# Optimization experiments

Hardware: AMD Instinct MI355X
Metric: run time of the kernel (lower is better)

Reference implementation:

```python
import jax, jax.numpy as jnp
import numpy as np

EMBED_DIM = 768
NUM_HEADS = 12
D_K = EMBED_DIM // NUM_HEADS
FFN_DIM = 3072
N_QUBITS = 8
LN_EPS = 1e-5


def layer_norm(x, g, b):
    mu = jnp.mean(x, axis=-1, keepdims=True)
    var = jnp.mean(jnp.square(x - mu), axis=-1, keepdims=True)
    return (x - mu) * jax.lax.rsqrt(var + LN_EPS) * g + b


def setup_inputs() -> dict:
    key = jax.random.key(0)
    ks = jax.random.split(key, 8)
    B, S = 4, 2048
    s_comb = 1.0 / np.sqrt(EMBED_DIM)
    s_w1 = 1.0 / np.sqrt(N_QUBITS)
    s_w2 = 1.0 / np.sqrt(FFN_DIM)
    return {
        "x": jax.random.normal(ks[0], (B, S, EMBED_DIM), jnp.float32),
        "combine_w": jax.random.uniform(ks[1], (EMBED_DIM, EMBED_DIM), jnp.float32, -s_comb, s_comb),
        "theta": jax.random.normal(ks[2], (N_QUBITS,), jnp.float32),
        "w1": jax.random.uniform(ks[3], (FFN_DIM, N_QUBITS), jnp.float32, -s_w1, s_w1),
        "w2": jax.random.uniform(ks[4], (EMBED_DIM, FFN_DIM), jnp.float32, -s_w2, s_w2),
        "ln1_g": jnp.ones((EMBED_DIM,), jnp.float32),
        "ln1_b": jnp.zeros((EMBED_DIM,), jnp.float32),
        "ln2_g": jnp.ones((EMBED_DIM,), jnp.float32),
        "ln2_b": jnp.zeros((EMBED_DIM,), jnp.float32),
    }


def reference(x, combine_w, theta, w1, w2, ln1_g, ln1_b, ln2_g, ln2_b):
    B, S, D = x.shape
    # --- attention (q = k = v = x split into heads; QLayer is never used in forward) ---
    xh = x.reshape(B, S, NUM_HEADS, D_K).transpose(0, 2, 1, 3)  # [B,H,S,dk]
    scores = jnp.einsum("bhqd,bhkd->bhqk", xh, xh) / jnp.sqrt(jnp.asarray(D_K, x.dtype))
    probs = jax.nn.softmax(scores, axis=-1)
    attn = jnp.einsum("bhqk,bhkd->bhqd", probs, xh)
    attn = attn.transpose(0, 2, 1, 3).reshape(B, S, D)
    attn_out = attn @ combine_w.T
    # --- residual + norm1 ---
    h = layer_norm(x + attn_out, ln1_g, ln1_b)
    # --- quantum FFN: RX(x_i) then RY(theta_i) per wire, <Z_i> = cos(x_i)*cos(theta_i) ---
    meas = jnp.cos(h[..., :N_QUBITS]) * jnp.cos(theta)  # [B,S,nq]
    ffn = jax.nn.relu(meas @ w1.T) @ w2.T               # [B,S,D]
    # --- residual + norm2 ---
    return layer_norm(h + ffn, ln2_g, ln2_b)
```

## Files before the change

kernel.cpp:

```cpp
#include <hip/hip_runtime.h>
#include <math.h>


#define B_    4
#define S_    2048
#define D_    768
#define H_    12
#define DK_   64
#define FFN_  3072
#define NQ_   8
#define M_    (B_ * S_)

typedef __attribute__((ext_vector_type(8))) short bf16x8;
typedef __attribute__((ext_vector_type(4))) float f32x4;

static __device__ __forceinline__ unsigned short f2bf(float f) {
    unsigned u = __float_as_uint(f);
    unsigned r = (u + 0x7FFFu + ((u >> 16) & 1u)) >> 16;
    return (unsigned short)r;
}
static __device__ __forceinline__ unsigned pk2(float a, float b) {
    return (unsigned)f2bf(a) | ((unsigned)f2bf(b) << 16);
}
static __device__ __forceinline__ bf16x8 pack8(float4 a, float4 b) {
    bf16x8 r;
    r[0] = (short)f2bf(a.x); r[1] = (short)f2bf(a.y);
    r[2] = (short)f2bf(a.z); r[3] = (short)f2bf(a.w);
    r[4] = (short)f2bf(b.x); r[5] = (short)f2bf(b.y);
    r[6] = (short)f2bf(b.z); r[7] = (short)f2bf(b.w);
    return r;
}

__global__ __launch_bounds__(256, 2)
void attn_mfma(const float* __restrict__ x, unsigned short* __restrict__ attnb)
{
    __shared__ __align__(16) short Ks[64 * 64];
    __shared__ __align__(16) short Vt[64 * 64];
    __shared__ __align__(16) short Ps[4 * 32 * 64];

    const int tid = threadIdx.x;
    const int w   = tid >> 6;
    const int l   = tid & 63;
    const int g   = l >> 4;
    const int l15 = l & 15;

    const int q0 = blockIdx.x * 128;
    const int hh = blockIdx.y;
    const int bb = blockIdx.z;

    const float* xh = x + ((size_t)bb * S_) * D_ + hh * DK_;

    bf16x8 qf[2][2];
    {
        const float* xq = xh + (size_t)(q0 + w * 32) * D_;
        #pragma unroll
        for (int qt = 0; qt < 2; ++qt)
            #pragma unroll
            for (int ks = 0; ks < 2; ++ks) {
                const float* p = xq + (size_t)(qt * 16 + l15) * D_ + ks * 32 + g * 8;
                float4 f0 = *reinterpret_cast<const float4*>(p);
                float4 f1 = *reinterpret_cast<const float4*>(p + 4);
                qf[qt][ks] = pack8(f0, f1);
            }
    }

    f32x4 oacc[2][4];
    float mrun[2][4], lrun[2][4];
    #pragma unroll
    for (int qt = 0; qt < 2; ++qt)
        #pragma unroll
        for (int i = 0; i < 4; ++i) {
            oacc[qt][i] = (f32x4){0.f, 0.f, 0.f, 0.f};
            mrun[qt][i] = -3.0e38f; lrun[qt][i] = 0.f;
        }

    short* Pw = Ps + w * 32 * 64;

    for (int kt = 0; kt < S_ / 64; ++kt) {
        __syncthreads();
        const float* xk = xh + (size_t)(kt * 64) * D_;

        #pragma unroll
        for (int it = 0; it < 2; ++it) {
            int c = tid + it * 256;
            int r = c >> 3, b = c & 7;
            const float* p = xk + (size_t)r * D_ + b * 8;
            float4 f0 = *reinterpret_cast<const float4*>(p);
            float4 f1 = *reinterpret_cast<const float4*>(p + 4);
            *reinterpret_cast<bf16x8*>(&Ks[r * 64 + ((b ^ (r & 7)) << 3)]) = pack8(f0, f1);
        }
        {
            int kv0 = (tid & 31) * 2;
            int dch = tid >> 5;
            unsigned* Vt32 = reinterpret_cast<unsigned*>(Vt);
            #pragma unroll
            for (int dp = 0; dp < 2; ++dp) {
                int d0 = dp * 32 + dch * 4;
                float4 fa = *reinterpret_cast<const float4*>(xk + (size_t)kv0 * D_ + d0);
                float4 fb = *reinterpret_cast<const float4*>(xk + (size_t)(kv0 + 1) * D_ + d0);
                const float* pa = reinterpret_cast<const float*>(&fa);
                const float* pb = reinterpret_cast<const float*>(&fb);
                #pragma unroll
                for (int j = 0; j < 4; ++j) {
                    int d = d0 + j;
                    Vt32[d * 32 + ((kv0 >> 1) ^ ((d & 7) << 2))] = pk2(pa[j], pb[j]);
                }
            }
        }
        __syncthreads();

        f32x4 sacc[2][4];
        #pragma unroll
        for (int qt = 0; qt < 2; ++qt)
            #pragma unroll
            for (int kj = 0; kj < 4; ++kj) sacc[qt][kj] = (f32x4){0.f, 0.f, 0.f, 0.f};

        #pragma unroll
        for (int ks = 0; ks < 2; ++ks) {
            bf16x8 kf[4];
            #pragma unroll
            for (int kj = 0; kj < 4; ++kj) {
                int r = kj * 16 + l15;
                kf[kj] = *reinterpret_cast<const bf16x8*>(
                    &Ks[r * 64 + (((ks * 4 + g) ^ (r & 7)) << 3)]);
            }
            #pragma unroll
            for (int qt = 0; qt < 2; ++qt)
                #pragma unroll
                for (int kj = 0; kj < 4; ++kj)
                    sacc[qt][kj] = __builtin_amdgcn_mfma_f32_16x16x32_bf16(
                        qf[qt][ks], kf[kj], sacc[qt][kj], 0, 0, 0);
        }

        #pragma unroll
        for (int qt = 0; qt < 2; ++qt) {
            #pragma unroll
            for (int reg = 0; reg < 4; ++reg) {
                float s0 = sacc[qt][0][reg] * 0.125f;
                float s1 = sacc[qt][1][reg] * 0.125f;
                float s2 = sacc[qt][2][reg] * 0.125f;
                float s3 = sacc[qt][3][reg] * 0.125f;
                float mx = fmaxf(fmaxf(s0, s1), fmaxf(s2, s3));
                #pragma unroll
                for (int msk = 1; msk < 16; msk <<= 1) mx = fmaxf(mx, __shfl_xor(mx, msk));
                float mnew = fmaxf(mrun[qt][reg], mx);
                float corr = __expf(mrun[qt][reg] - mnew);
                mrun[qt][reg] = mnew;
                float p0 = __expf(s0 - mnew), p1 = __expf(s1 - mnew);
                float p2 = __expf(s2 - mnew), p3 = __expf(s3 - mnew);
                float ps = (p0 + p1) + (p2 + p3);
                #pragma unroll
                for (int msk = 1; msk < 16; msk <<= 1) ps += __shfl_xor(ps, msk);
                lrun[qt][reg] = lrun[qt][reg] * corr + ps;
                #pragma unroll
                for (int dt = 0; dt < 4; ++dt) oacc[qt][dt][reg] *= corr;
                int q = qt * 16 + g * 4 + reg;
                short* pr = Pw + q * 64;
                int sw = (q & 7) << 3;
                pr[(0 * 16 + l15) ^ sw] = (short)f2bf(p0);
                pr[(1 * 16 + l15) ^ sw] = (short)f2bf(p1);
                pr[(2 * 16 + l15) ^ sw] = (short)f2bf(p2);
                pr[(3 * 16 + l15) ^ sw] = (short)f2bf(p3);
            }
        }

        #pragma unroll
        for (int ks = 0; ks < 2; ++ks) {
            bf16x8 pf[2], vf[4];
            #pragma unroll
            for (int qt = 0; qt < 2; ++qt) {
                int q = qt * 16 + l15;
                pf[qt] = *reinterpret_cast<const bf16x8*>(
                    &Pw[q * 64 + (((ks * 4 + g) ^ (q & 7)) << 3)]);
            }
            #pragma unroll
            for (int dt = 0; dt < 4; ++dt) {
                int d = dt * 16 + l15;
                vf[dt] = *reinterpret_cast<const bf16x8*>(
                    &Vt[d * 64 + (((ks * 4 + g) ^ (d & 7)) << 3)]);
            }
            #pragma unroll
            for (int qt = 0; qt < 2; ++qt)
                #pragma unroll
                for (int dt = 0; dt < 4; ++dt)
                    oacc[qt][dt] = __builtin_amdgcn_mfma_f32_16x16x32_bf16(
                        pf[qt], vf[dt], oacc[qt][dt], 0, 0, 0);
        }
    }

    unsigned short* ao = attnb + ((size_t)bb * S_ + q0 + w * 32) * D_ + hh * DK_;
    #pragma unroll
    for (int qt = 0; qt < 2; ++qt)
        #pragma unroll
        for (int reg = 0; reg < 4; ++reg) {
            int q = qt * 16 + g * 4 + reg;
            float inv = 1.0f / lrun[qt][reg];
            unsigned short* rp = ao + (size_t)q * D_;
            #pragma unroll
            for (int dt = 0; dt < 4; ++dt)
                rp[dt * 16 + l15] = f2bf(oacc[qt][dt][reg] * inv);
        }
}

__global__ __launch_bounds__(256, 2)
void gemm_combine(const unsigned short* __restrict__ A, const float* __restrict__ W,
                  const float* __restrict__ xres, float* __restrict__ y1)
{
    __shared__ __align__(16) short As[128 * 64];
    __shared__ __align__(16) short Bs[128 * 64];

    const int tid = threadIdx.x;
    const int w = tid >> 6, l = tid & 63, g = l >> 4, l15 = l & 15;
    const int wr = w >> 1, wc = w & 1;
    const int m0 = blockIdx.x * 128, n0 = blockIdx.y * 128;

    f32x4 acc[4][4];
    #pragma unroll
    for (int i = 0; i < 4; ++i)
        #pragma unroll
        for (int j = 0; j < 4; ++j) acc[i][j] = (f32x4){0.f, 0.f, 0.f, 0.f};

    for (int k0 = 0; k0 < D_; k0 += 64) {
        __syncthreads();
        #pragma unroll
        for (int it = 0; it < 4; ++it) {
            int c = tid + it * 256;
            int r = c >> 3, b = c & 7;
            bf16x8 v = *reinterpret_cast<const bf16x8*>(
                A + (size_t)(m0 + r) * D_ + k0 + b * 8);
            *reinterpret_cast<bf16x8*>(&As[r * 64 + ((b ^ (r & 7)) << 3)]) = v;
        }
        #pragma unroll
        for (int it = 0; it < 4; ++it) {
            int c = tid + it * 256;
            int r = c >> 3, b = c & 7;
            const float* p = W + (size_t)(n0 + r) * D_ + k0 + b * 8;
            float4 f0 = *reinterpret_cast<const float4*>(p);
            float4 f1 = *reinterpret_cast<const float4*>(p + 4);
            *reinterpret_cast<bf16x8*>(&Bs[r * 64 + ((b ^ (r & 7)) << 3)]) = pack8(f0, f1);
        }
        __syncthreads();

        #pragma unroll
        for (int ks = 0; ks < 2; ++ks) {
            bf16x8 af[4], bf[4];
            #pragma unroll
            for (int mt = 0; mt < 4; ++mt) {
                int r = wr * 64 + mt * 16 + l15;
                af[mt] = *reinterpret_cast<const bf16x8*>(
                    &As[r * 64 + (((ks * 4 + g) ^ (r & 7)) << 3)]);
            }
            #pragma unroll
            for (int nt = 0; nt < 4; ++nt) {
                int cc = wc * 64 + nt * 16 + l15;
                bf[nt] = *reinterpret_cast<const bf16x8*>(
                    &Bs[cc * 64 + (((ks * 4 + g) ^ (cc & 7)) << 3)]);
            }
            #pragma unroll
            for (int mt = 0; mt < 4; ++mt)
                #pragma unroll
                for (int nt = 0; nt < 4; ++nt)
                    acc[mt][nt] = __builtin_amdgcn_mfma_f32_16x16x32_bf16(
                        af[mt], bf[nt], acc[mt][nt], 0, 0, 0);
        }
    }

    #pragma unroll
    for (int mt = 0; mt < 4; ++mt)
        #pragma unroll
        for (int reg = 0; reg < 4; ++reg) {
            size_t row = (size_t)m0 + wr * 64 + mt * 16 + g * 4 + reg;
            #pragma unroll
            for (int nt = 0; nt < 4; ++nt) {
                int col = n0 + wc * 64 + nt * 16 + l15;
                y1[row * D_ + col] = acc[mt][nt][reg] + xres[row * D_ + col];
            }
        }
}

__global__ __launch_bounds__(256, 2)
void ffn_mfma(const float* __restrict__ hin, const float* __restrict__ theta,
              const float* __restrict__ w1, const float* __restrict__ w2,
              float* __restrict__ y2)
{
    __shared__ __align__(16) short Ts[128 * 64];
    __shared__ __align__(16) short Bs[128 * 64];
    __shared__ float meas_s[128][9];

    const int tid = threadIdx.x;
    const int w = tid >> 6, l = tid & 63, g = l >> 4, l15 = l & 15;
    const int wr = w >> 1, wc = w & 1;
    const int m0 = blockIdx.x * 128, n0 = blockIdx.y * 128;

    if (tid < 128) {
        const float* hp = hin + (size_t)(m0 + tid) * D_;
        #pragma unroll
        for (int q = 0; q < NQ_; ++q)
            meas_s[tid][q] = cosf(hp[q]) * cosf(theta[q]);
    }

    const int cp   = tid & 31;
    const int rblk = tid >> 5;
    unsigned* Ts32 = reinterpret_cast<unsigned*>(Ts);

    f32x4 acc[4][4];
    #pragma unroll
    for (int i = 0; i < 4; ++i)
        #pragma unroll
        for (int j = 0; j < 4; ++j) acc[i][j] = (f32x4){0.f, 0.f, 0.f, 0.f};

    for (int k0 = 0; k0 < FFN_; k0 += 64) {
        __syncthreads();
        #pragma unroll
        for (int it = 0; it < 4; ++it) {
            int c = tid + it * 256;
            int r = c >> 3, b = c & 7;
            const float* p = w2 + (size_t)(n0 + r) * FFN_ + k0 + b * 8;
            float4 f0 = *reinterpret_cast<const float4*>(p);
            float4 f1 = *reinterpret_cast<const float4*>(p + 4);
            *reinterpret_cast<bf16x8*>(&Bs[r * 64 + ((b ^ (r & 7)) << 3)]) = pack8(f0, f1);
        }
        {
            const float* wA = w1 + (size_t)(k0 + 2 * cp) * NQ_;
            const float* wB = wA + NQ_;
            float4 a0 = *reinterpret_cast<const float4*>(wA);
            float4 a1 = *reinterpret_cast<const float4*>(wA + 4);
            float4 b0 = *reinterpret_cast<const float4*>(wB);
            float4 b1 = *reinterpret_cast<const float4*>(wB + 4);
            const float* wAa = reinterpret_cast<const float*>(&a0);
            const float* wAb = reinterpret_cast<const float*>(&a1);
            const float* wBa = reinterpret_cast<const float*>(&b0);
            const float* wBb = reinterpret_cast<const float*>(&b1);
            #pragma unroll
            for (int i = 0; i < 16; ++i) {
                int r = rblk * 16 + i;
                float t0 = 0.f, t1 = 0.f;
                #pragma unroll
                for (int q = 0; q < 4; ++q) {
                    float m = meas_s[r][q];
                    t0 = fmaf(m, wAa[q], t0);
                    t1 = fmaf(m, wBa[q], t1);
                }
                #pragma unroll
                for (int q = 0; q < 4; ++q) {
                    float m = meas_s[r][q + 4];
                    t0 = fmaf(m, wAb[q], t0);
                    t1 = fmaf(m, wBb[q], t1);
                }
                t0 = fmaxf(t0, 0.f); t1 = fmaxf(t1, 0.f);
                Ts32[r * 32 + (cp ^ ((r & 7) << 2))] = pk2(t0, t1);
            }
        }
        __syncthreads();

        #pragma unroll
        for (int ks = 0; ks < 2; ++ks) {
            bf16x8 af[4], bf[4];
            #pragma unroll
            for (int mt = 0; mt < 4; ++mt) {
                int r = wr * 64 + mt * 16 + l15;
                af[mt] = *reinterpret_cast<const bf16x8*>(
                    &Ts[r * 64 + (((ks * 4 + g) ^ (r & 7)) << 3)]);
            }
            #pragma unroll
            for (int nt = 0; nt < 4; ++nt) {
                int cc = wc * 64 + nt * 16 + l15;
                bf[nt] = *reinterpret_cast<const bf16x8*>(
                    &Bs[cc * 64 + (((ks * 4 + g) ^ (cc & 7)) << 3)]);
            }
            #pragma unroll
            for (int mt = 0; mt < 4; ++mt)
                #pragma unroll
                for (int nt = 0; nt < 4; ++nt)
                    acc[mt][nt] = __builtin_amdgcn_mfma_f32_16x16x32_bf16(
                        af[mt], bf[nt], acc[mt][nt], 0, 0, 0);
        }
    }

    #pragma unroll
    for (int mt = 0; mt < 4; ++mt)
        #pragma unroll
        for (int reg = 0; reg < 4; ++reg) {
            size_t row = (size_t)m0 + wr * 64 + mt * 16 + g * 4 + reg;
            #pragma unroll
            for (int nt = 0; nt < 4; ++nt) {
                int col = n0 + wc * 64 + nt * 16 + l15;
                y2[row * D_ + col] = acc[mt][nt][reg] + hin[row * D_ + col];
            }
        }
}

__global__ __launch_bounds__(256, 4)
void ln_kernel(const float* __restrict__ in, const float* __restrict__ g,
               const float* __restrict__ bt, float* __restrict__ out)
{
    const int wave = threadIdx.x >> 6, lane = threadIdx.x & 63;
    const size_t row = (size_t)blockIdx.x * 4 + wave;
    const float* p = in + row * D_;
    float v[12];
    float sum = 0.f;
    #pragma unroll
    for (int c = 0; c < 3; ++c) {
        float4 f = *reinterpret_cast<const float4*>(p + (c * 64 + lane) * 4);
        v[c*4+0] = f.x; v[c*4+1] = f.y; v[c*4+2] = f.z; v[c*4+3] = f.w;
        sum += (f.x + f.y) + (f.z + f.w);
    }
    #pragma unroll
    for (int msk = 1; msk < 64; msk <<= 1) sum += __shfl_xor(sum, msk);
    const float mu = sum * (1.0f / 768.0f);
    float vs = 0.f;
    #pragma unroll
    for (int k = 0; k < 12; ++k) { float d = v[k] - mu; vs = fmaf(d, d, vs); }
    #pragma unroll
    for (int msk = 1; msk < 64; msk <<= 1) vs += __shfl_xor(vs, msk);
    const float rstd = rsqrtf(vs * (1.0f / 768.0f) + 1e-5f);
    float* po = out + row * D_;
    #pragma unroll
    for (int c = 0; c < 3; ++c) {
        const int base = (c * 64 + lane) * 4;
        float4 gg = *reinterpret_cast<const float4*>(g + base);
        float4 bb2 = *reinterpret_cast<const float4*>(bt + base);
        float4 r;
        r.x = (v[c*4+0] - mu) * rstd * gg.x + bb2.x;
        r.y = (v[c*4+1] - mu) * rstd * gg.y + bb2.y;
        r.z = (v[c*4+2] - mu) * rstd * gg.z + bb2.z;
        r.w = (v[c*4+3] - mu) * rstd * gg.w + bb2.w;
        *reinterpret_cast<float4*>(po + base) = r;
    }
}

extern "C" void kernel_launch(void* const* d_in, const int* in_sizes, int n_in,
                              void* d_out, int out_size, void* d_ws, size_t ws_size,
                              hipStream_t stream)
{
    const float* x   = (const float*)d_in[0];
    const float* cw  = (const float*)d_in[1];
    const float* th  = (const float*)d_in[2];
    const float* w1  = (const float*)d_in[3];
    const float* w2  = (const float*)d_in[4];
    const float* g1  = (const float*)d_in[5];
    const float* b1  = (const float*)d_in[6];
    const float* g2  = (const float*)d_in[7];
    const float* b2  = (const float*)d_in[8];
    float* out = (float*)d_out;

    const size_t NE = (size_t)M_ * D_;
    float* ws = (float*)d_ws;
    unsigned short* attnb = (unsigned short*)ws;
    float* hbuf = ws + NE;
    float* y1   = out;
    float* y2   = ws;

    attn_mfma   <<<dim3(S_ / 128, H_, B_), 256, 0, stream>>>(x, attnb);
    gemm_combine<<<dim3(M_ / 128, D_ / 128), 256, 0, stream>>>(attnb, cw, x, y1);
    ln_kernel   <<<dim3(M_ / 4), 256, 0, stream>>>(y1, g1, b1, hbuf);
    ffn_mfma    <<<dim3(M_ / 128, D_ / 128), 256, 0, stream>>>(hbuf, th, w1, w2, y2);
    ln_kernel   <<<dim3(M_ / 4), 256, 0, stream>>>(y2, g2, b2, out);
}
```

Baseline: 543.9 us.

## Widen attention KV tile, pre-convert weights to bf16, split FFN into T-build plus LDS-DMA GEMM

The attention kernel now processes 128 keys per iteration and rescales only when the running max increases. Combine and W2 weights are converted to bf16 once per call by a new kernel, and a new templated GEMM loads A and B tiles straight into LDS with global_load_lds. The fused FFN is split: a tbuild kernel materializes relu(meas@w1ᵀ) as a bf16 [M,3072] buffer, and the generic GEMM consumes it. This aims to stop each FFN block from recomputing the hidden activations and converting fp32 weights, at the cost of extra workspace traffic (about 50 MB for T) and two more launches. The old path is kept as a fallback when the workspace is too small.

Measured after the change: 579.4 us. +6.5%, slower.

```diff
diff --git a/kernel.cpp b/kernel.cpp
--- a/kernel.cpp
+++ b/kernel.cpp
@@ -19,6 +19,9 @@
     unsigned r = (u + 0x7FFFu + ((u >> 16) & 1u)) >> 16;
     return (unsigned short)r;
 }
+static __device__ __forceinline__ float bf2f(unsigned short h) {
+    return __uint_as_float((unsigned)h << 16);
+}
 static __device__ __forceinline__ unsigned pk2(float a, float b) {
     return (unsigned)f2bf(a) | ((unsigned)f2bf(b) << 16);
 }
@@ -31,12 +34,26 @@
     return r;
 }
 
+#define CWCH 73728
+#define W2CH 294912
+__global__ void convert_w(const float* __restrict__ cw, const float* __restrict__ w2,
+                          unsigned short* __restrict__ cwb, unsigned short* __restrict__ w2b)
+{
+    int idx = blockIdx.x * 256 + threadIdx.x;
+    const float* src; unsigned short* dst; int c;
+    if (idx < CWCH) { src = cw; dst = cwb; c = idx; }
+    else            { src = w2; dst = w2b; c = idx - CWCH; if (c >= W2CH) return; }
+    float4 f0 = *reinterpret_cast<const float4*>(src + (size_t)c * 8);
+    float4 f1 = *reinterpret_cast<const float4*>(src + (size_t)c * 8 + 4);
+    *reinterpret_cast<bf16x8*>(dst + (size_t)c * 8) = pack8(f0, f1);
+}
+
 __global__ __launch_bounds__(256, 2)
 void attn_mfma(const float* __restrict__ x, unsigned short* __restrict__ attnb)
 {
-    __shared__ __align__(16) short Ks[64 * 64];
-    __shared__ __align__(16) short Vt[64 * 64];
-    __shared__ __align__(16) short Ps[4 * 32 * 64];
+    __shared__ __align__(16) short    Ks[128 * 64];
+    __shared__ __align__(16) unsigned Vt32[64 * 64];
+    __shared__ __align__(16) short    Ps[4][32 * 128];
 
     const int tid = threadIdx.x;
     const int w   = tid >> 6;
@@ -74,14 +91,14 @@
             mrun[qt][i] = -3.0e38f; lrun[qt][i] = 0.f;
         }
 
-    short* Pw = Ps + w * 32 * 64;
-
-    for (int kt = 0; kt < S_ / 64; ++kt) {
-        __syncthreads();
-        const float* xk = xh + (size_t)(kt * 64) * D_;
-
-        #pragma unroll
-        for (int it = 0; it < 2; ++it) {
+    short* Pw = Ps[w];
+
+    for (int kt = 0; kt < S_ / 128; ++kt) {
+        __syncthreads();
+        const float* xk = xh + (size_t)(kt * 128) * D_;
+
+        #pragma unroll
+        for (int it = 0; it < 4; ++it) {
             int c = tid + it * 256;
             int r = c >> 3, b = c & 7;
             const float* p = xk + (size_t)r * D_ + b * 8;
@@ -90,36 +107,38 @@
             *reinterpret_cast<bf16x8*>(&Ks[r * 64 + ((b ^ (r & 7)) << 3)]) = pack8(f0, f1);
         }
         {
-            int kv0 = (tid & 31) * 2;
-            int dch = tid >> 5;
-            unsigned* Vt32 = reinterpret_cast<unsigned*>(Vt);
-            #pragma unroll
-            for (int dp = 0; dp < 2; ++dp) {
-                int d0 = dp * 32 + dch * 4;
-                float4 fa = *reinterpret_cast<const float4*>(xk + (size_t)kv0 * D_ + d0);
-                float4 fb = *reinterpret_cast<const float4*>(xk + (size_t)(kv0 + 1) * D_ + d0);
-                const float* pa = reinterpret_cast<const float*>(&fa);
-                const float* pb = reinterpret_cast<const float*>(&fb);
-                #pragma unroll
-                for (int j = 0; j < 4; ++j) {
-                    int d = d0 + j;
-                    Vt32[d * 32 + ((kv0 >> 1) ^ ((d & 7) << 2))] = pk2(pa[j], pb[j]);
-                }
-            }
-        }
-        __syncthreads();
-
-        f32x4 sacc[2][4];
+            int kvp = tid & 63;
+            int dg  = tid >> 6;
+            const float* ra = xk + (size_t)(2 * kvp) * D_ + dg * 16;
+            const float* rb = ra + D_;
+            float va[16], vb[16];
+            *reinterpret_cast<float4*>(&va[0])  = *reinterpret_cast<const float4*>(ra);
+            *reinterpret_cast<float4*>(&va[4])  = *reinterpret_cast<const float4*>(ra + 4);
+            *reinterpret_cast<float4*>(&va[8])  = *reinterpret_cast<const float4*>(ra + 8);
+            *reinterpret_cast<float4*>(&va[12]) = *reinterpret_cast<const float4*>(ra + 12);
+            *reinterpret_cast<float4*>(&vb[0])  = *reinterpret_cast<const float4*>(rb);
+            *reinterpret_cast<float4*>(&vb[4])  = *reinterpret_cast<const float4*>(rb + 4);
+            *reinterpret_cast<float4*>(&vb[8])  = *reinterpret_cast<const float4*>(rb + 8);
+            *reinterpret_cast<float4*>(&vb[12]) = *reinterpret_cast<const float4*>(rb + 12);
+            #pragma unroll
+            for (int j = 0; j < 16; ++j) {
+                int d = dg * 16 + j;
+                Vt32[d * 64 + (kvp ^ ((d & 7) << 2))] = pk2(va[j], vb[j]);
+            }
+        }
+        __syncthreads();
+
+        f32x4 sacc[2][8];
         #pragma unroll
         for (int qt = 0; qt < 2; ++qt)
             #pragma unroll
-            for (int kj = 0; kj < 4; ++kj) sacc[qt][kj] = (f32x4){0.f, 0.f, 0.f, 0.f};
+            for (int kj = 0; kj < 8; ++kj) sacc[qt][kj] = (f32x4){0.f, 0.f, 0.f, 0.f};
 
         #pragma unroll
         for (int ks = 0; ks < 2; ++ks) {
-            bf16x8 kf[4];
-            #pragma unroll
-            for (int kj = 0; kj < 4; ++kj) {
+            bf16x8 kf[8];
+            #pragma unroll
+            for (int kj = 0; kj < 8; ++kj) {
                 int r = kj * 16 + l15;
                 kf[kj] = *reinterpret_cast<const bf16x8*>(
                     &Ks[r * 64 + (((ks * 4 + g) ^ (r & 7)) << 3)]);
@@ -127,7 +146,7 @@
             #pragma unroll
             for (int qt = 0; qt < 2; ++qt)
                 #pragma unroll
-                for (int kj = 0; kj < 4; ++kj)
+                for (int kj = 0; kj < 8; ++kj)
                     sacc[qt][kj] = __builtin_amdgcn_mfma_f32_16x16x32_bf16(
                         qf[qt][ks], kf[kj], sacc[qt][kj], 0, 0, 0);
         }
@@ -136,48 +155,54 @@
         for (int qt = 0; qt < 2; ++qt) {
             #pragma unroll
             for (int reg = 0; reg < 4; ++reg) {
-                float s0 = sacc[qt][0][reg] * 0.125f;
-                float s1 = sacc[qt][1][reg] * 0.125f;
-                float s2 = sacc[qt][2][reg] * 0.125f;
-                float s3 = sacc[qt][3][reg] * 0.125f;
-                float mx = fmaxf(fmaxf(s0, s1), fmaxf(s2, s3));
+                float sv[8];
+                #pragma unroll
+                for (int kj = 0; kj < 8; ++kj) sv[kj] = sacc[qt][kj][reg] * 0.125f;
+                float mx = fmaxf(fmaxf(fmaxf(sv[0], sv[1]), fmaxf(sv[2], sv[3])),
+                                 fmaxf(fmaxf(sv[4], sv[5]), fmaxf(sv[6], sv[7])));
                 #pragma unroll
                 for (int msk = 1; msk < 16; msk <<= 1) mx = fmaxf(mx, __shfl_xor(mx, msk));
-                float mnew = fmaxf(mrun[qt][reg], mx);
-                float corr = __expf(mrun[qt][reg] - mnew);
-                mrun[qt][reg] = mnew;
-                float p0 = __expf(s0 - mnew), p1 = __expf(s1 - mnew);
-                float p2 = __expf(s2 - mnew), p3 = __expf(s3 - mnew);
-                float ps = (p0 + p1) + (p2 + p3);
-                #pragma unroll
-                for (int msk = 1; msk < 16; msk <<= 1) ps += __shfl_xor(ps, msk);
-                lrun[qt][reg] = lrun[qt][reg] * corr + ps;
-                #pragma unroll
-                for (int dt = 0; dt < 4; ++dt) oacc[qt][dt][reg] *= corr;
+                float mold = mrun[qt][reg];
+                if (mx > mold) {
+                    float corr = __expf(mold - mx);
+                    lrun[qt][reg] *= corr;
+                    #pragma unroll
+                    for (int dt = 0; dt < 4; ++dt) oacc[qt][dt][reg] *= corr;
+                    mrun[qt][reg] = mx;
+                }
+                float mcur = mrun[qt][reg];
                 int q = qt * 16 + g * 4 + reg;
-                short* pr = Pw + q * 64;
-                int sw = (q & 7) << 3;
-                pr[(0 * 16 + l15) ^ sw] = (short)f2bf(p0);
-                pr[(1 * 16 + l15) ^ sw] = (short)f2bf(p1);
-                pr[(2 * 16 + l15) ^ sw] = (short)f2bf(p2);
-                pr[(3 * 16 + l15) ^ sw] = (short)f2bf(p3);
-            }
-        }
-
-        #pragma unroll
-        for (int ks = 0; ks < 2; ++ks) {
+                short* pr = Pw + q * 128;
+                int qs = q & 7;
+                float psum = 0.f;
+                #pragma unroll
+                for (int kj = 0; kj < 8; ++kj) {
+                    float p = __expf(sv[kj] - mcur);
+                    psum += p;
+                    int c  = kj * 16 + l15;
+                    int ch = c >> 3;
+                    pr[((ch ^ qs) << 3) | (c & 7)] = (short)f2bf(p);
+                }
+                #pragma unroll
+                for (int msk = 1; msk < 16; msk <<= 1) psum += __shfl_xor(psum, msk);
+                lrun[qt][reg] += psum;
+            }
+        }
+
+        #pragma unroll
+        for (int ks = 0; ks < 4; ++ks) {
             bf16x8 pf[2], vf[4];
             #pragma unroll
             for (int qt = 0; qt < 2; ++qt) {
                 int q = qt * 16 + l15;
                 pf[qt] = *reinterpret_cast<const bf16x8*>(
-                    &Pw[q * 64 + (((ks * 4 + g) ^ (q & 7)) << 3)]);
+                    &Pw[q * 128 + (((ks * 4 + g) ^ (q & 7)) << 3)]);
             }
             #pragma unroll
             for (int dt = 0; dt < 4; ++dt) {
                 int d = dt * 16 + l15;
                 vf[dt] = *reinterpret_cast<const bf16x8*>(
-                    &Vt[d * 64 + (((ks * 4 + g) ^ (d & 7)) << 3)]);
+                    &Vt32[d * 64 + ((ks * 16 + g * 4) ^ ((d & 7) << 2))]);
             }
             #pragma unroll
             for (int qt = 0; qt < 2; ++qt)
@@ -202,13 +227,173 @@
         }
 }
 
+template<int KDIM>
 __global__ __launch_bounds__(256, 2)
-void gemm_combine(const unsigned short* __restrict__ A, const float* __restrict__ W,
-                  const float* __restrict__ xres, float* __restrict__ y1)
+void gemm_bf16(const unsigned short* __restrict__ A, const unsigned short* __restrict__ Bw,
+               const float* __restrict__ res, float* __restrict__ out)
 {
     __shared__ __align__(16) short As[128 * 64];
     __shared__ __align__(16) short Bs[128 * 64];
 
+    const int tid = threadIdx.x;
+    const int w = tid >> 6, l = tid & 63, g = l >> 4, l15 = l & 15;
+    const int wr = w >> 1, wc = w & 1;
+    const int m0 = blockIdx.x * 128, n0 = blockIdx.y * 128;
+
+    f32x4 acc[4][4];
+    #pragma unroll
+    for (int i = 0; i < 4; ++i)
+        #pragma unroll
+        for (int j = 0; j < 4; ++j) acc[i][j] = (f32x4){0.f, 0.f, 0.f, 0.f};
+
+    for (int k0 = 0; k0 < KDIM; k0 += 64) {
+        __syncthreads();
+        #pragma unroll
+        for (int it = 0; it < 4; ++it) {
+            int c = tid + it * 256;
+            int r = c >> 3, b = c & 7;
+            int ldsbase = (it * 256 + w * 64) << 3;
+            const unsigned short* ga = A + (size_t)(m0 + r) * KDIM + k0 + ((b ^ (r & 7)) << 3);
+            __builtin_amdgcn_global_load_lds(
+                (const __attribute__((address_space(1))) void*)ga,
+                (__attribute__((address_space(3))) void*)(As + ldsbase), 16, 0, 0);
+            const unsigned short* gb = Bw + (size_t)(n0 + r) * KDIM + k0 + ((b ^ (r & 7)) << 3);
+            __builtin_amdgcn_global_load_lds(
+                (const __attribute__((address_space(1))) void*)gb,
+                (__attribute__((address_space(3))) void*)(Bs + ldsbase), 16, 0, 0);
+        }
+        __syncthreads();
+
+        #pragma unroll
+        for (int ks = 0; ks < 2; ++ks) {
+            bf16x8 af[4], bf[4];
+            #pragma unroll
+            for (int mt = 0; mt < 4; ++mt) {
+                int r = wr * 64 + mt * 16 + l15;
+                af[mt] = *reinterpret_cast<const bf16x8*>(
+                    &As[r * 64 + (((ks * 4 + g) ^ (r & 7)) << 3)]);
+            }
+            #pragma unroll
+            for (int nt = 0; nt < 4; ++nt) {
+                int cc = wc * 64 + nt * 16 + l15;
+                bf[nt] = *reinterpret_cast<const bf16x8*>(
+                    &Bs[cc * 64 + (((ks * 4 + g) ^ (cc & 7)) << 3)]);
+            }
+            #pragma unroll
+            for (int mt = 0; mt < 4; ++mt)
+                #pragma unroll
+                for (int nt = 0; nt < 4; ++nt)
+                    acc[mt][nt] = __builtin_amdgcn_mfma_f32_16x16x32_bf16(
+                        af[mt], bf[nt], acc[mt][nt], 0, 0, 0);
+        }
+    }
+
+    #pragma unroll
+    for (int mt = 0; mt < 4; ++mt)
+        #pragma unroll
+        for (int reg = 0; reg < 4; ++reg) {
+            size_t row = (size_t)m0 + wr * 64 + mt * 16 + g * 4 + reg;
+            #pragma unroll
+            for (int nt = 0; nt < 4; ++nt) {
+                int col = n0 + wc * 64 + nt * 16 + l15;
+                out[row * D_ + col] = acc[mt][nt][reg] + res[row * D_ + col];
+            }
+        }
+}
+
+__global__ __launch_bounds__(256, 2)
+void tbuild(const float* __restrict__ h, const float* __restrict__ theta,
+            const float* __restrict__ w1, unsigned short* __restrict__ Tb)
+{
+    __shared__ __align__(16) short w1s[FFN_ * NQ_];
+
+    const int tid = threadIdx.x;
+    const int w = tid >> 6, l = tid & 63;
+
+    #pragma unroll
+    for (int it = 0; it < 12; ++it) {
+        int c = tid + it * 256;
+        float4 f0 = *reinterpret_cast<const float4*>(w1 + (size_t)c * 8);
+        float4 f1 = *reinterpret_cast<const float4*>(w1 + (size_t)c * 8 + 4);
+        *reinterpret_cast<bf16x8*>(&w1s[c * 8]) = pack8(f0, f1);
+    }
+    __syncthreads();
+
+    float cth[NQ_];
+    #pragma unroll
+    for (int q = 0; q < NQ_; ++q) cth[q] = cosf(theta[q]);
+
+    #pragma unroll
+    for (int rr = 0; rr < 4; ++rr) {
+        int row = blockIdx.x * 16 + w * 4 + rr;
+        const float* hp = h + (size_t)row * D_;
+        float meas[NQ_];
+        #pragma unroll
+        for (int q = 0; q < NQ_; ++q) meas[q] = cosf(hp[q]) * cth[q];
+        unsigned short* outp = Tb + (size_t)row * FFN_;
+        #pragma unroll
+        for (int itc = 0; itc < 6; ++itc) {
+            int cbase = itc * 512 + l * 8;
+            bf16x8 tv;
+            #pragma unroll
+            for (int cc = 0; cc < 8; ++cc) {
+                bf16x8 wv = *reinterpret_cast<const bf16x8*>(&w1s[(cbase + cc) * 8]);
+                float t = 0.f;
+                #pragma unroll
+                for (int q = 0; q < NQ_; ++q)
+                    t = fmaf(meas[q], bf2f((unsigned short)wv[q]), t);
+                tv[cc] = (short)f2bf(fmaxf(t, 0.f));
+            }
+            *reinterpret_cast<bf16x8*>(&outp[cbase]) = tv;
+        }
+    }
+}
+
+__global__ __launch_bounds__(256, 4)
+void ln_kernel(const float* __restrict__ in, const float* __restrict__ g,
+               const float* __restrict__ bt, float* __restrict__ out)
+{
+    const int wave = threadIdx.x >> 6, lane = threadIdx.x & 63;
+    const size_t row = (size_t)blockIdx.x * 4 + wave;
+    const float* p = in + row * D_;
+    float v[12];
+    float sum = 0.f;
+    #pragma unroll
+    for (int c = 0; c < 3; ++c) {
+        float4 f = *reinterpret_cast<const float4*>(p + (c * 64 + lane) * 4);
+        v[c*4+0] = f.x; v[c*4+1] = f.y; v[c*4+2] = f.z; v[c*4+3] = f.w;
+        sum += (f.x + f.y) + (f.z + f.w);
+    }
+    #pragma unroll
+    for (int msk = 1; msk < 64; msk <<= 1) sum += __shfl_xor(sum, msk);
+    const float mu = sum * (1.0f / 768.0f);
+    float vs = 0.f;
+    #pragma unroll
+    for (int k = 0; k < 12; ++k) { float d = v[k] - mu; vs = fmaf(d, d, vs); }
+    #pragma unroll
+    for (int msk = 1; msk < 64; msk <<= 1) vs += __shfl_xor(vs, msk);
+    const float rstd = rsqrtf(vs * (1.0f / 768.0f) + 1e-5f);
+    float* po = out + row * D_;
+    #pragma unroll
+    for (int c = 0; c < 3; ++c) {
+        const int base = (c * 64 + lane) * 4;
+        float4 gg = *reinterpret_cast<const float4*>(g + base);
+        float4 bb2 = *reinterpret_cast<const float4*>(bt + base);
+        float4 r;
+        r.x = (v[c*4+0] - mu) * rstd * gg.x + bb2.x;
+        r.y = (v[c*4+1] - mu) * rstd * gg.y + bb2.y;
+        r.z = (v[c*4+2] - mu) * rstd * gg.z + bb2.z;
+        r.w = (v[c*4+3] - mu) * rstd * gg.w + bb2.w;
+        *reinterpret_cast<float4*>(po + base) = r;
+    }
+}
+
+__global__ __launch_bounds__(256, 2)
+void gemm_combine_f32w(const unsigned short* __restrict__ A, const float* __restrict__ W,
+                       const float* __restrict__ xres, float* __restrict__ y1)
+{
+    __shared__ __align__(16) short As[128 * 64];
+    __shared__ __align__(16) short Bs[128 * 64];
     const int tid = threadIdx.x;
     const int w = tid >> 6, l = tid & 63, g = l >> 4, l15 = l & 15;
     const int wr = w >> 1, wc = w & 1;
@@ -229,18 +414,12 @@
             bf16x8 v = *reinterpret_cast<const bf16x8*>(
                 A + (size_t)(m0 + r) * D_ + k0 + b * 8);
             *reinterpret_cast<bf16x8*>(&As[r * 64 + ((b ^ (r & 7)) << 3)]) = v;
-        }
-        #pragma unroll
-        for (int it = 0; it < 4; ++it) {
-            int c = tid + it * 256;
-            int r = c >> 3, b = c & 7;
             const float* p = W + (size_t)(n0 + r) * D_ + k0 + b * 8;
             float4 f0 = *reinterpret_cast<const float4*>(p);
             float4 f1 = *reinterpret_cast<const float4*>(p + 4);
             *reinterpret_cast<bf16x8*>(&Bs[r * 64 + ((b ^ (r & 7)) << 3)]) = pack8(f0, f1);
         }
         __syncthreads();
-
         #pragma unroll
         for (int ks = 0; ks < 2; ++ks) {
             bf16x8 af[4], bf[4];
@@ -264,7 +443,6 @@
                         af[mt], bf[nt], acc[mt][nt], 0, 0, 0);
         }
     }
-
     #pragma unroll
     for (int mt = 0; mt < 4; ++mt)
         #pragma unroll
@@ -279,9 +457,9 @@
 }
 
 __global__ __launch_bounds__(256, 2)
-void ffn_mfma(const float* __restrict__ hin, const float* __restrict__ theta,
-              const float* __restrict__ w1, const float* __restrict__ w2,
-              float* __restrict__ y2)
+void ffn_fused(const float* __restrict__ hin, const float* __restrict__ theta,
+               const float* __restrict__ w1, const float* __restrict__ w2,
+               float* __restrict__ y2)
 {
     __shared__ __align__(16) short Ts[128 * 64];
     __shared__ __align__(16) short Bs[128 * 64];
@@ -352,7 +530,6 @@
             }
         }
         __syncthreads();
-
         #pragma unroll
         for (int ks = 0; ks < 2; ++ks) {
             bf16x8 af[4], bf[4];
@@ -376,7 +553,6 @@
                         af[mt], bf[nt], acc[mt][nt], 0, 0, 0);
         }
     }
-
     #pragma unroll
     for (int mt = 0; mt < 4; ++mt)
         #pragma unroll
@@ -388,45 +564,6 @@
                 y2[row * D_ + col] = acc[mt][nt][reg] + hin[row * D_ + col];
             }
         }
-}
-
-__global__ __launch_bounds__(256, 4)
-void ln_kernel(const float* __restrict__ in, const float* __restrict__ g,
-               const float* __restrict__ bt, float* __restrict__ out)
-{
-    const int wave = threadIdx.x >> 6, lane = threadIdx.x & 63;
-    const size_t row = (size_t)blockIdx.x * 4 + wave;
-    const float* p = in + row * D_;
-    float v[12];
-    float sum = 0.f;
-    #pragma unroll
-    for (int c = 0; c < 3; ++c) {
-        float4 f = *reinterpret_cast<const float4*>(p + (c * 64 + lane) * 4);
-        v[c*4+0] = f.x; v[c*4+1] = f.y; v[c*4+2] = f.z; v[c*4+3] = f.w;
-        sum += (f.x + f.y) + (f.z + f.w);
-    }
-    #pragma unroll
-    for (int msk = 1; msk < 64; msk <<= 1) sum += __shfl_xor(sum, msk);
-    const float mu = sum * (1.0f / 768.0f);
-    float vs = 0.f;
-    #pragma unroll
-    for (int k = 0; k < 12; ++k) { float d = v[k] - mu; vs = fmaf(d, d, vs); }
-    #pragma unroll
-    for (int msk = 1; msk < 64; msk <<= 1) vs += __shfl_xor(vs, msk);
-    const float rstd = rsqrtf(vs * (1.0f / 768.0f) + 1e-5f);
-    float* po = out + row * D_;
-    #pragma unroll
-    for (int c = 0; c < 3; ++c) {
-        const int base = (c * 64 + lane) * 4;
-        float4 gg = *reinterpret_cast<const float4*>(g + base);
-        float4 bb2 = *reinterpret_cast<const float4*>(bt + base);
-        float4 r;
-        r.x = (v[c*4+0] - mu) * rstd * gg.x + bb2.x;
-        r.y = (v[c*4+1] - mu) * rstd * gg.y + bb2.y;
-        r.z = (v[c*4+2] - mu) * rstd * gg.z + bb2.z;
-        r.w = (v[c*4+3] - mu) * rstd * gg.w + bb2.w;
-        *reinterpret_cast<float4*>(po + base) = r;
-    }
 }
 
 extern "C" void kernel_launch(void* const* d_in, const int* in_sizes, int n_in,
@@ -444,16 +581,37 @@
     const float* b2  = (const float*)d_in[8];
     float* out = (float*)d_out;
 
-    const size_t NE = (size_t)M_ * D_;
-    float* ws = (float*)d_ws;
-    unsigned short* attnb = (unsigned short*)ws;
-    float* hbuf = ws + NE;
-    float* y1   = out;
-    float* y2   = ws;
-
-    attn_mfma   <<<dim3(S_ / 128, H_, B_), 256, 0, stream>>>(x, attnb);
-    gemm_combine<<<dim3(M_ / 128, D_ / 128), 256, 0, stream>>>(attnb, cw, x, y1);
-    ln_kernel   <<<dim3(M_ / 4), 256, 0, stream>>>(y1, g1, b1, hbuf);
-    ffn_mfma    <<<dim3(M_ / 128, D_ / 128), 256, 0, stream>>>(hbuf, th, w1, w2, y2);
-    ln_kernel   <<<dim3(M_ / 4), 256, 0, stream>>>(y2, g2, b2, out);
-}
+    const size_t HB  = 25165824;
+    const size_t TBB = 50331648;
+    const size_t CWB = 1179648;
+    const size_t WS_NEED = HB + TBB + CWB + 4718592;
+
+    if (ws_size >= WS_NEED) {
+        char* wsc = (char*)d_ws;
+        float*          hbuf  = (float*)wsc;
+        unsigned short* attnb = (unsigned short*)(wsc + HB);
+        unsigned short* Tb    = (unsigned short*)(wsc + HB);
+        unsigned short* cwb   = (unsigned short*)(wsc + HB + TBB);
+        unsigned short* w2b   = (unsigned short*)(wsc + HB + TBB + CWB);
+
+        convert_w      <<<dim3((CWCH + W2CH) / 256), 256, 0, stream>>>(cw, w2, cwb, w2b);
+        attn_mfma      <<<dim3(S_ / 128, H_, B_), 256, 0, stream>>>(x, attnb);
+        gemm_bf16<D_>  <<<dim3(M_ / 128, D_ / 128), 256, 0, stream>>>(attnb, cwb, x, out);
+        ln_kernel      <<<dim3(M_ / 4), 256, 0, stream>>>(out, g1, b1, hbuf);
+        tbuild         <<<dim3(M_ / 16), 256, 0, stream>>>(hbuf, th, w1, Tb);
+        gemm_bf16<FFN_><<<dim3(M_ / 128, D_ / 128), 256, 0, stream>>>(Tb, w2b, hbuf, out);
+        ln_kernel      <<<dim3(M_ / 4), 256, 0, stream>>>(out, g2, b2, out);
+    } else {
+        const size_t NE = (size_t)M_ * D_;
+        float* ws = (float*)d_ws;
+        unsigned short* attnb = (unsigned short*)ws;
+        float* hbuf = ws + NE;
+        float* y2   = ws;
+
+        attn_mfma       <<<dim3(S_ / 128, H_, B_), 256, 0, stream>>>(x, attnb);
+        gemm_combine_f32w<<<dim3(M_ / 128, D_ / 128), 256, 0, stream>>>(attnb, cw, x, out);
+        ln_kernel       <<<dim3(M_ / 4), 256, 0, stream>>>(out, g1, b1, hbuf);
+        ffn_fused       <<<dim3(M_ / 128, D_ / 128), 256, 0, stream>>>(hbuf, th, w1, w2, y2);
+        ln_kernel       <<<dim3(M_ / 4), 256, 0, stream>>>(y2, g2, b2, out);
+    }
+}
```
